# Kernel tuning notes

Measured on AMD Instinct MI355X. Metric: run time of the kernel, lower is better.

## Reference

```python
import jax, jax.numpy as jnp
import numpy as np

TAU = 2.0  # LIF membrane time constant (spikingjelly default)
SCALE = 0.125

@jax.custom_vjp
def heaviside(x):
    return (x >= 0).astype(x.dtype)

def _hv_fwd(x):
    return heaviside(x), x

def _hv_bwd(x, g):
    s = jax.nn.sigmoid(4.0 * x)  # sigmoid surrogate, alpha=4
    return (g * 4.0 * s * (1.0 - s),)

heaviside.defvjp(_hv_fwd, _hv_bwd)

def lif(x, v_th):
    """Multi-step LIF over leading time axis. x: [T, ...]. decay_input, hard reset to 0."""
    def step(v, xt):
        v = v + (xt - v) / TAU
        s = heaviside(v - v_th)
        return v * (1.0 - s), s
    return jax.lax.scan(step, jnp.zeros_like(x[0]), x)[1]

def conv1x1(x, w, b=None):
    # x: [T,B,C,N], w: [O,C]
    y = jnp.einsum('oc,tbcn->tbon', w, x)
    if b is not None:
        y = y + b[None, None, :, None]
    return y

def bn(x, p, eps=1e-5):
    # inference-mode BatchNorm1d over channel axis; p: [4,C] = gamma,beta,mean,var
    g, b, m, v = p[0], p[1], p[2], p[3]
    inv = g / jnp.sqrt(v + eps)
    return x * inv[None, None, :, None] + (b - m * inv)[None, None, :, None]

def setup_inputs() -> dict:
    key = jax.random.key(0)
    ks = jax.random.split(key, 10)
    T, B, C, H, W = 4, 32, 512, 16, 16
    wscale = 1.0 / np.sqrt(C)
    def bn_params(k):
        k1, k2, k3, k4 = jax.random.split(k, 4)
        gamma = 1.0 + 0.1 * jax.random.normal(k1, (C,))
        beta = 0.1 * jax.random.normal(k2, (C,))
        mean = 0.1 * jax.random.normal(k3, (C,))
        var = 1.0 + 0.1 * jax.random.uniform(k4, (C,))
        return jnp.stack([gamma, beta, mean, var])
    return {
        'x': jax.random.normal(ks[0], (T, B, C, H, W), dtype=jnp.float32),
        'res_attn': jnp.zeros((1,), dtype=jnp.float32),
        'q_w': wscale * jax.random.normal(ks[1], (C, C), dtype=jnp.float32),
        'k_w': wscale * jax.random.normal(ks[2], (C, C), dtype=jnp.float32),
        'v_w': wscale * jax.random.normal(ks[3], (C, C), dtype=jnp.float32),
        'proj_w': wscale * jax.random.normal(ks[4], (C, C), dtype=jnp.float32),
        'proj_b': 0.01 * jax.random.normal(ks[5], (C,), dtype=jnp.float32),
        'q_bn': bn_params(ks[6]),
        'k_bn': bn_params(ks[7]),
        'v_bn': bn_params(ks[8]),
        'p_bn': bn_params(ks[9]),
    }

def reference(x, res_attn, q_w, k_w, v_w, proj_w, proj_b, q_bn, k_bn, v_bn, p_bn):
    T, B, C, H, W = x.shape
    num_heads = 8
    d = C // num_heads
    N = H * W
    xf = x.reshape(T, B, C, N)

    def branch(w, p, v_th):
        return lif(bn(conv1x1(xf, w), p), v_th)

    def to_heads(t):  # [T,B,C,N] -> [T,B,h,N,d]
        return t.transpose(0, 1, 3, 2).reshape(T, B, N, num_heads, d).transpose(0, 1, 3, 2, 4)

    q = to_heads(branch(q_w, q_bn, 1.0))
    k = to_heads(branch(k_w, k_bn, 1.0))
    v = to_heads(branch(v_w, v_bn, 1.0))

    # linear (non-softmax) attention: q @ (k^T @ v) * scale
    kv = jnp.einsum('tbhnd,tbhne->tbhde', k, v)
    a = jnp.einsum('tbhnd,tbhde->tbhne', q, kv) * SCALE  # [T,B,h,N,d]

    # [T,B,h,N,d] -> transpose(3,4) -> [T,B,h,d,N] -> [T,B,C,N]
    a = jnp.swapaxes(a, 3, 4).reshape(T, B, C, N)
    a = lif(a, 0.5)  # attn_lif with v_threshold=0.5

    out = conv1x1(a, proj_w, proj_b)
    out = bn(out, p_bn).reshape(T, B, C, H, W)
    out = lif(out, 1.0)
    return out, v
```

## Files before the change

### kernel.cpp

```cpp
#include <hip/hip_runtime.h>
#include <stdint.h>

#define T_ 4
#define B_ 32
#define C_ 512
#define N_ 256
#define NH_ 8
#define NB_ (N_ / 8)
#define BITS_BYTES_ ((size_t)(T_ * B_ * C_) * NB_)

typedef float f32x2 __attribute__((ext_vector_type(2)));


__global__ __launch_bounds__(256, 2) void qkv_gemm_lif(
    const float* __restrict__ x, const float* __restrict__ wq,
    const float* __restrict__ wk, const float* __restrict__ wv,
    const float* __restrict__ bnq, const float* __restrict__ bnk,
    const float* __restrict__ bnv,
    uint8_t* __restrict__ sbits, float* __restrict__ out1) {
#pragma clang fp contract(off)
  const int br = blockIdx.z;
  const int b  = blockIdx.y;
  const int ot = blockIdx.x >> 1, nt = blockIdx.x & 1;
  const float* w = (br == 0) ? wq : (br == 1) ? wk : wv;
  const float* bn = (br == 0) ? bnq : (br == 1) ? bnk : bnv;
  uint8_t* sb = sbits + (size_t)br * BITS_BYTES_;

  const int tid = threadIdx.x;
  const int tx = tid & 15, ty = tid >> 4;
  const int o0 = ot * 64, n0 = nt * 128;

  __shared__ float As[16][64];
  __shared__ float Bs[16][128];

  float inv[4], add[4];
#pragma unroll
  for (int i = 0; i < 4; ++i) {
    int o = o0 + ty * 4 + i;
    float g = bn[o], be = bn[C_ + o], mm = bn[2 * C_ + o], va = bn[3 * C_ + o];
    float iv = g / sqrtf(va + 1e-5f);
    inv[i] = iv;
    add[i] = be - mm * iv;
  }

  float vst[4][8];
#pragma unroll
  for (int i = 0; i < 4; ++i)
#pragma unroll
    for (int j = 0; j < 8; ++j) vst[i][j] = 0.f;

  for (int t = 0; t < T_; ++t) {
    const float* xb = x + (size_t)(t * B_ + b) * (C_ * N_);
    f32x2 acc2[4][4];
#pragma unroll
    for (int i = 0; i < 4; ++i)
#pragma unroll
      for (int jp = 0; jp < 4; ++jp) acc2[i][jp] = (f32x2){0.f, 0.f};

    for (int kc = 0; kc < C_; kc += 16) {
      int o = tid & 63, kq = (tid >> 6) * 4;
      float4 a4 = *(const float4*)(w + (size_t)(o0 + o) * C_ + kc + kq);
      int fr = tid >> 5, fq = (tid & 31) * 4;
      int fr2 = (tid + 256) >> 5, fq2 = ((tid + 256) & 31) * 4;
      float4 b40 = *(const float4*)(xb + (size_t)(kc + fr) * N_ + n0 + fq);
      float4 b41 = *(const float4*)(xb + (size_t)(kc + fr2) * N_ + n0 + fq2);
      __syncthreads();
      As[kq + 0][o] = a4.x; As[kq + 1][o] = a4.y;
      As[kq + 2][o] = a4.z; As[kq + 3][o] = a4.w;
      *(float4*)(&Bs[fr][fq]) = b40;
      *(float4*)(&Bs[fr2][fq2]) = b41;
      __syncthreads();
#pragma unroll
      for (int k = 0; k < 16; ++k) {
        float4 av4 = *(const float4*)(&As[k][ty * 4]);
        float4 bq0 = *(const float4*)(&Bs[k][tx * 4]);
        float4 bq1 = *(const float4*)(&Bs[k][64 + tx * 4]);
        f32x2 b2[4];
        b2[0] = (f32x2){bq0.x, bq0.y}; b2[1] = (f32x2){bq0.z, bq0.w};
        b2[2] = (f32x2){bq1.x, bq1.y}; b2[3] = (f32x2){bq1.z, bq1.w};
        float av[4] = {av4.x, av4.y, av4.z, av4.w};
#pragma unroll
        for (int i = 0; i < 4; ++i) {
          f32x2 ai = (f32x2){av[i], av[i]};
#pragma unroll
          for (int jp = 0; jp < 4; ++jp) {
            f32x2 p = ai * b2[jp];
            acc2[i][jp] = acc2[i][jp] + p;
          }
        }
      }
    }
    __syncthreads();

    {
      size_t tb = (size_t)(t * B_ + b);
      unsigned nibsA = 0, nibsB = 0;
#pragma unroll
      for (int i = 0; i < 4; ++i) {
#pragma unroll
        for (int jj = 0; jj < 8; ++jj) {
          float a = acc2[i][jj >> 1][jj & 1];
          float y0 = a * inv[i];
          float y = y0 + add[i];
          float d = y - vst[i][jj];
          float vs = vst[i][jj] + d * 0.5f;
          unsigned sp = (vs >= 1.0f) ? 1u : 0u;
          vst[i][jj] = sp ? 0.f : vs;
          if (jj < 4) nibsA |= sp << (4 * i + jj);
          else        nibsB |= sp << (4 * i + jj - 4);
        }
      }
      unsigned oA = __shfl_xor(nibsA, 1);
      unsigned oB = __shfl_xor(nibsB, 1);
      int m = tx >> 1;
      if ((tx & 1) == 0) {
#pragma unroll
        for (int i = 0; i < 4; ++i) {
          int o = o0 + ty * 4 + i;
          unsigned byte_ = ((nibsA >> (4 * i)) & 0xF) | (((oA >> (4 * i)) & 0xF) << 4);
          sb[(tb * C_ + o) * NB_ + (n0 >> 3) + m] = (uint8_t)byte_;
        }
      } else {
#pragma unroll
        for (int i = 0; i < 4; ++i) {
          int o = o0 + ty * 4 + i;
          unsigned byte_ = ((oB >> (4 * i)) & 0xF) | (((nibsB >> (4 * i)) & 0xF) << 4);
          sb[(tb * C_ + o) * NB_ + (n0 >> 3) + 8 + m] = (uint8_t)byte_;
        }
      }
      if (br == 2) {
#pragma unroll
        for (int i = 0; i < 4; ++i) {
          int o = o0 + ty * 4 + i;
          int h = o >> 6, dd = o & 63;
          size_t base = ((tb * NH_ + h) * (size_t)N_) * 64 + dd;
#pragma unroll
          for (int jj = 0; jj < 8; ++jj) {
            int n = n0 + ((jj < 4) ? (tx * 4 + jj) : (64 + tx * 4 + jj - 4));
            unsigned sp = (jj < 4) ? ((nibsA >> (4 * i + jj)) & 1u)
                                   : ((nibsB >> (4 * i + jj - 4)) & 1u);
            out1[base + (size_t)n * 64] = sp ? 1.0f : 0.0f;
          }
        }
      }
    }
  }
}

__global__ __launch_bounds__(512, 1) void attn_lif(
    const uint8_t* __restrict__ bits, uint8_t* __restrict__ abits) {
#pragma clang fp contract(off)
  const unsigned long long* qb = (const unsigned long long*)bits;
  const unsigned long long* kb = qb + BITS_BYTES_ / 8;
  const unsigned long long* vb = kb + BITS_BYTES_ / 8;
  unsigned long long* ap = (unsigned long long*)abits;

  const int h = blockIdx.x, b = blockIdx.y;
  const int tid = threadIdx.x;
  const int lane = tid & 63, wave = tid >> 6;
  const int nw = wave & 3, eh = wave >> 2;

  __shared__ unsigned long long kbl[64][4];
  __shared__ unsigned long long vbl[64][4];
  __shared__ float kvl[64][64];

  float state[32];
#pragma unroll
  for (int e = 0; e < 32; ++e) state[e] = 0.f;

  for (int t = 0; t < T_; ++t) {
    size_t row0 = (size_t)(t * B_ + b) * C_ + h * 64;
    {
      int i = tid & 255, c = i >> 2, w = i & 3;
      if (tid < 256) kbl[c][w] = kb[(row0 + c) * 4 + w];
      else           vbl[c][w] = vb[(row0 + c) * 4 + w];
    }
    __syncthreads();
    {
      int d = tid & 63, eb = (tid >> 6) * 8;
#pragma unroll
      for (int e2 = 0; e2 < 8; ++e2) {
        int e = eb + e2;
        int s = 0;
#pragma unroll
        for (int w = 0; w < 4; ++w) s += __popcll(kbl[d][w] & vbl[e][w]);
        kvl[d][e] = (float)s;
      }
    }
    __syncthreads();
    float acc[32];
#pragma unroll
    for (int e = 0; e < 32; ++e) acc[e] = 0.f;
    for (int d = 0; d < 64; ++d) {
      unsigned long long qw = qb[(row0 + d) * 4 + nw];
      float qf = (float)(unsigned)((qw >> lane) & 1ULL);
      const float* kr = &kvl[d][eh * 32];
#pragma unroll
      for (int e = 0; e < 32; ++e) acc[e] = acc[e] + qf * kr[e];
    }
    {
#pragma unroll
      for (int e2 = 0; e2 < 32; ++e2) {
        int e = eh * 32 + e2;
        float a = acc[e2] * 0.125f;
        float d0 = a - state[e2];
        float vs = state[e2] + d0 * 0.5f;
        int sp = (vs >= 0.5f) ? 1 : 0;
        state[e2] = sp ? 0.f : vs;
        unsigned long long m = __ballot(sp);
        if (lane == 0) ap[(row0 + e) * 4 + nw] = m;
      }
    }
    __syncthreads();
  }
}

__global__ __launch_bounds__(256, 2) void proj_gemm_lif(
    const uint8_t* __restrict__ ab, const float* __restrict__ wp,
    const float* __restrict__ pb, const float* __restrict__ bnp,
    float* __restrict__ out0) {
  const int b = blockIdx.y;
  const int ot = blockIdx.x >> 1, nt = blockIdx.x & 1;
  const int tid = threadIdx.x;
  const int tx = tid & 15, ty = tid >> 4;
  const int o0 = ot * 64, n0 = nt * 128;

  __shared__ float As[16][64];
  __shared__ float Bs[16][128];

  float inv[4], add[4], bias[4];
  {
#pragma clang fp contract(off)
#pragma unroll
    for (int i = 0; i < 4; ++i) {
      int o = o0 + ty * 4 + i;
      float g = bnp[o], be = bnp[C_ + o], mm = bnp[2 * C_ + o], va = bnp[3 * C_ + o];
      float iv = g / sqrtf(va + 1e-5f);
      inv[i] = iv;
      add[i] = be - mm * iv;
      bias[i] = pb[o];
    }
  }

  float vst[4][8];
#pragma unroll
  for (int i = 0; i < 4; ++i)
#pragma unroll
    for (int j = 0; j < 8; ++j) vst[i][j] = 0.f;

  for (int t = 0; t < T_; ++t) {
    f32x2 acc2[4][4];
#pragma unroll
    for (int i = 0; i < 4; ++i)
#pragma unroll
      for (int jp = 0; jp < 4; ++jp) acc2[i][jp] = (f32x2){0.f, 0.f};
    size_t tb = (size_t)(t * B_ + b);

    for (int kc = 0; kc < C_; kc += 16) {
      {
        int o = tid & 63, kq = (tid >> 6) * 4;
        float4 a4 = *(const float4*)(wp + (size_t)(o0 + o) * C_ + kc + kq);
        As[kq + 0][o] = a4.x; As[kq + 1][o] = a4.y;
        As[kq + 2][o] = a4.z; As[kq + 3][o] = a4.w;
      }
      {
        int r = tid >> 4, q16 = tid & 15;
        uint8_t by = ab[(tb * C_ + kc + r) * NB_ + (n0 >> 3) + q16];
        int nb = q16 * 8;
#pragma unroll
        for (int j = 0; j < 8; ++j) Bs[r][nb + j] = (float)((by >> j) & 1);
      }
      __syncthreads();
#pragma unroll
      for (int k = 0; k < 16; ++k) {
        float4 av4 = *(const float4*)(&As[k][ty * 4]);
        float4 bq0 = *(const float4*)(&Bs[k][tx * 4]);
        float4 bq1 = *(const float4*)(&Bs[k][64 + tx * 4]);
        f32x2 b2[4];
        b2[0] = (f32x2){bq0.x, bq0.y}; b2[1] = (f32x2){bq0.z, bq0.w};
        b2[2] = (f32x2){bq1.x, bq1.y}; b2[3] = (f32x2){bq1.z, bq1.w};
        float av[4] = {av4.x, av4.y, av4.z, av4.w};
#pragma unroll
        for (int i = 0; i < 4; ++i) {
          f32x2 ai = (f32x2){av[i], av[i]};
#pragma unroll
          for (int jp = 0; jp < 4; ++jp)
            acc2[i][jp] = acc2[i][jp] + ai * b2[jp];
        }
      }
      __syncthreads();
    }

    {
#pragma clang fp contract(off)
#pragma unroll
      for (int i = 0; i < 4; ++i) {
        int o = o0 + ty * 4 + i;
        float4 r0, r1;
#pragma unroll
        for (int jj = 0; jj < 8; ++jj) {
          float a = acc2[i][jj >> 1][jj & 1];
          float y1 = a + bias[i];
          float y2 = y1 * inv[i];
          float y = y2 + add[i];
          float d0 = y - vst[i][jj];
          float vs = vst[i][jj] + d0 * 0.5f;
          int sp = (vs >= 1.0f) ? 1 : 0;
          vst[i][jj] = sp ? 0.f : vs;
          if (jj < 4) (&r0.x)[jj] = sp ? 1.0f : 0.0f;
          else        (&r1.x)[jj - 4] = sp ? 1.0f : 0.0f;
        }
        float* dst = out0 + (tb * C_ + o) * N_ + n0;
        *(float4*)(dst + tx * 4) = r0;
        *(float4*)(dst + 64 + tx * 4) = r1;
      }
    }
  }
}


extern "C" void kernel_launch(void* const* d_in, const int* in_sizes, int n_in,
                              void* d_out, int out_size, void* d_ws, size_t ws_size,
                              hipStream_t stream) {
  const float* x   = (const float*)d_in[0];
  const float* qw  = (const float*)d_in[2];
  const float* kw  = (const float*)d_in[3];
  const float* vw  = (const float*)d_in[4];
  const float* pw  = (const float*)d_in[5];
  const float* pbb = (const float*)d_in[6];
  const float* qbn = (const float*)d_in[7];
  const float* kbn = (const float*)d_in[8];
  const float* vbn = (const float*)d_in[9];
  const float* pbn = (const float*)d_in[10];

  uint8_t* bits  = (uint8_t*)d_ws;
  uint8_t* abits = bits + 3 * BITS_BYTES_;

  float* out0 = (float*)d_out;
  float* out1 = out0 + (size_t)T_ * B_ * C_ * N_;

  qkv_gemm_lif<<<dim3(16, 32, 3), dim3(256), 0, stream>>>(
      x, qw, kw, vw, qbn, kbn, vbn, bits, out1);
  attn_lif<<<dim3(8, 32), dim3(512), 0, stream>>>(bits, abits);
  proj_gemm_lif<<<dim3(16, 32), dim3(256), 0, stream>>>(abits, pw, pbb, pbn,
                                                        out0);
}
```

Baseline: 1.375 ms.

## Enlarge QKV GEMM block tile to 128x128 with 8x8 outputs per thread

The QKV GEMM+LIF kernel now covers 128 output channels per block instead of 64, so each thread computes an 8x8 micro-tile. The grid is halved along the output dimension. Each staged tile of x in shared memory is now reused across twice as many output channels, and the ratio of shared-memory loads to FMAs improves. In exchange, register pressure rises (64 accumulators plus 64 LIF states), the occupancy hint of two blocks per CU is dropped, and fewer blocks are launched.

```diff
diff --git a/kernel.cpp b/kernel.cpp
--- a/kernel.cpp
+++ b/kernel.cpp
@@ -12,7 +12,7 @@
 typedef float f32x2 __attribute__((ext_vector_type(2)));
 
 
-__global__ __launch_bounds__(256, 2) void qkv_gemm_lif(
+__global__ __launch_bounds__(256) void qkv_gemm_lif(
     const float* __restrict__ x, const float* __restrict__ wq,
     const float* __restrict__ wk, const float* __restrict__ wv,
     const float* __restrict__ bnq, const float* __restrict__ bnk,
@@ -28,59 +28,66 @@
 
   const int tid = threadIdx.x;
   const int tx = tid & 15, ty = tid >> 4;
-  const int o0 = ot * 64, n0 = nt * 128;
-
-  __shared__ float As[16][64];
+  const int o0 = ot * 128, n0 = nt * 128;
+
+  __shared__ float As[16][128];
   __shared__ float Bs[16][128];
 
-  float inv[4], add[4];
-#pragma unroll
-  for (int i = 0; i < 4; ++i) {
-    int o = o0 + ty * 4 + i;
+  float inv[8], add[8];
+#pragma unroll
+  for (int i = 0; i < 8; ++i) {
+    int orel = (i < 4) ? (ty * 4 + i) : (64 + ty * 4 + i - 4);
+    int o = o0 + orel;
     float g = bn[o], be = bn[C_ + o], mm = bn[2 * C_ + o], va = bn[3 * C_ + o];
     float iv = g / sqrtf(va + 1e-5f);
     inv[i] = iv;
     add[i] = be - mm * iv;
   }
 
-  float vst[4][8];
-#pragma unroll
-  for (int i = 0; i < 4; ++i)
+  float vst[8][8];
+#pragma unroll
+  for (int i = 0; i < 8; ++i)
 #pragma unroll
     for (int j = 0; j < 8; ++j) vst[i][j] = 0.f;
+
+  const int ao = tid & 127, ah = tid >> 7;
+  const int fr = tid >> 5, fq = (tid & 31) * 4;
+  const int fr2 = 8 + fr;
 
   for (int t = 0; t < T_; ++t) {
     const float* xb = x + (size_t)(t * B_ + b) * (C_ * N_);
-    f32x2 acc2[4][4];
-#pragma unroll
-    for (int i = 0; i < 4; ++i)
+    f32x2 acc2[8][4];
+#pragma unroll
+    for (int i = 0; i < 8; ++i)
 #pragma unroll
       for (int jp = 0; jp < 4; ++jp) acc2[i][jp] = (f32x2){0.f, 0.f};
 
     for (int kc = 0; kc < C_; kc += 16) {
-      int o = tid & 63, kq = (tid >> 6) * 4;
-      float4 a4 = *(const float4*)(w + (size_t)(o0 + o) * C_ + kc + kq);
-      int fr = tid >> 5, fq = (tid & 31) * 4;
-      int fr2 = (tid + 256) >> 5, fq2 = ((tid + 256) & 31) * 4;
+      const float* wrow = w + (size_t)(o0 + ao) * C_ + kc + ah * 8;
+      float4 a0 = *(const float4*)(wrow);
+      float4 a1 = *(const float4*)(wrow + 4);
       float4 b40 = *(const float4*)(xb + (size_t)(kc + fr) * N_ + n0 + fq);
-      float4 b41 = *(const float4*)(xb + (size_t)(kc + fr2) * N_ + n0 + fq2);
+      float4 b41 = *(const float4*)(xb + (size_t)(kc + fr2) * N_ + n0 + fq);
       __syncthreads();
-      As[kq + 0][o] = a4.x; As[kq + 1][o] = a4.y;
-      As[kq + 2][o] = a4.z; As[kq + 3][o] = a4.w;
+      As[ah * 8 + 0][ao] = a0.x; As[ah * 8 + 1][ao] = a0.y;
+      As[ah * 8 + 2][ao] = a0.z; As[ah * 8 + 3][ao] = a0.w;
+      As[ah * 8 + 4][ao] = a1.x; As[ah * 8 + 5][ao] = a1.y;
+      As[ah * 8 + 6][ao] = a1.z; As[ah * 8 + 7][ao] = a1.w;
       *(float4*)(&Bs[fr][fq]) = b40;
-      *(float4*)(&Bs[fr2][fq2]) = b41;
+      *(float4*)(&Bs[fr2][fq]) = b41;
       __syncthreads();
 #pragma unroll
       for (int k = 0; k < 16; ++k) {
-        float4 av4 = *(const float4*)(&As[k][ty * 4]);
+        float4 aq0 = *(const float4*)(&As[k][ty * 4]);
+        float4 aq1 = *(const float4*)(&As[k][64 + ty * 4]);
         float4 bq0 = *(const float4*)(&Bs[k][tx * 4]);
         float4 bq1 = *(const float4*)(&Bs[k][64 + tx * 4]);
         f32x2 b2[4];
         b2[0] = (f32x2){bq0.x, bq0.y}; b2[1] = (f32x2){bq0.z, bq0.w};
         b2[2] = (f32x2){bq1.x, bq1.y}; b2[3] = (f32x2){bq1.z, bq1.w};
-        float av[4] = {av4.x, av4.y, av4.z, av4.w};
-#pragma unroll
-        for (int i = 0; i < 4; ++i) {
+        float av[8] = {aq0.x, aq0.y, aq0.z, aq0.w, aq1.x, aq1.y, aq1.z, aq1.w};
+#pragma unroll
+        for (int i = 0; i < 8; ++i) {
           f32x2 ai = (f32x2){av[i], av[i]};
 #pragma unroll
           for (int jp = 0; jp < 4; ++jp) {
@@ -96,7 +103,7 @@
       size_t tb = (size_t)(t * B_ + b);
       unsigned nibsA = 0, nibsB = 0;
 #pragma unroll
-      for (int i = 0; i < 4; ++i) {
+      for (int i = 0; i < 8; ++i) {
 #pragma unroll
         for (int jj = 0; jj < 8; ++jj) {
           float a = acc2[i][jj >> 1][jj & 1];
@@ -115,23 +122,26 @@
       int m = tx >> 1;
       if ((tx & 1) == 0) {
 #pragma unroll
-        for (int i = 0; i < 4; ++i) {
-          int o = o0 + ty * 4 + i;
+        for (int i = 0; i < 8; ++i) {
+          int orel = (i < 4) ? (ty * 4 + i) : (64 + ty * 4 + i - 4);
+          int o = o0 + orel;
           unsigned byte_ = ((nibsA >> (4 * i)) & 0xF) | (((oA >> (4 * i)) & 0xF) << 4);
           sb[(tb * C_ + o) * NB_ + (n0 >> 3) + m] = (uint8_t)byte_;
         }
       } else {
 #pragma unroll
-        for (int i = 0; i < 4; ++i) {
-          int o = o0 + ty * 4 + i;
+        for (int i = 0; i < 8; ++i) {
+          int orel = (i < 4) ? (ty * 4 + i) : (64 + ty * 4 + i - 4);
+          int o = o0 + orel;
           unsigned byte_ = ((oB >> (4 * i)) & 0xF) | (((nibsB >> (4 * i)) & 0xF) << 4);
           sb[(tb * C_ + o) * NB_ + (n0 >> 3) + 8 + m] = (uint8_t)byte_;
         }
       }
       if (br == 2) {
 #pragma unroll
-        for (int i = 0; i < 4; ++i) {
-          int o = o0 + ty * 4 + i;
+        for (int i = 0; i < 8; ++i) {
+          int orel = (i < 4) ? (ty * 4 + i) : (64 + ty * 4 + i - 4);
+          int o = o0 + orel;
           int h = o >> 6, dd = o & 63;
           size_t base = ((tb * NH_ + h) * (size_t)N_) * 64 + dd;
 #pragma unroll
@@ -339,7 +349,7 @@
   float* out0 = (float*)d_out;
   float* out1 = out0 + (size_t)T_ * B_ * C_ * N_;
 
-  qkv_gemm_lif<<<dim3(16, 32, 3), dim3(256), 0, stream>>>(
+  qkv_gemm_lif<<<dim3(8, 32, 3), dim3(256), 0, stream>>>(
       x, qw, kw, vw, qbn, kbn, vbn, bits, out1);
   attn_lif<<<dim3(8, 32), dim3(512), 0, stream>>>(bits, abits);
   proj_gemm_lif<<<dim3(16, 32), dim3(256), 0, stream>>>(abits, pw, pbb, pbn,
```

Measured after the change: 1.763 ms. 28.2% more time.
